# Performance work log

Measured on AMD Instinct MI355X. Metric: run time of the kernel, lower is better.

Reference implementation:

```python
import jax, jax.numpy as jnp
import numpy as np

D = 1024
H = 16
HD = D // H
EPS = 1e-6


def rms_norm(x, w):
    # x: [..., hd]; compute in float32 like the torch module
    xf = x.astype(jnp.float32)
    rms = jnp.sqrt(jnp.mean(xf * xf, axis=-1, keepdims=True) + EPS)
    return (xf / rms * w.astype(jnp.float32)).astype(x.dtype)


def setup_inputs() -> dict:
    key = jax.random.key(0)
    ks = jax.random.split(key, 6)
    B, S = 2, 2048
    x = jax.random.normal(ks[0], (B, S, D), dtype=jnp.float32)
    Wqkv = jax.random.normal(ks[1], (3 * D, D), dtype=jnp.float32) * (1.0 / np.sqrt(D))
    bqkv = jax.random.normal(ks[2], (3 * D,), dtype=jnp.float32) * 0.02
    Wproj = jax.random.normal(ks[3], (D, D), dtype=jnp.float32) * (1.0 / np.sqrt(D))
    bproj = jax.random.normal(ks[4], (D,), dtype=jnp.float32) * 0.02
    qn_w = jnp.ones((HD,), dtype=jnp.float32)
    kn_w = jnp.ones((HD,), dtype=jnp.float32)
    return {"x": x, "Wqkv": Wqkv, "bqkv": bqkv, "Wproj": Wproj, "bproj": bproj,
            "qn_w": qn_w, "kn_w": kn_w}


def reference(x, Wqkv, bqkv, Wproj, bproj, qn_w, kn_w):
    B, S, _ = x.shape
    # QKV projection: torch Linear is x @ W.T + b
    qkv = x @ Wqkv.T + bqkv                     # [B, S, 3D]
    qkv = qkv.reshape(B, S, 3, H, HD)
    q, k, v = qkv[:, :, 0], qkv[:, :, 1], qkv[:, :, 2]   # each [B, S, H, hd]
    q = rms_norm(q, qn_w)
    k = rms_norm(k, kn_w)
    # move heads forward: [B, H, S, hd]
    q = q.transpose(0, 2, 1, 3)
    k = k.transpose(0, 2, 1, 3)
    v = v.transpose(0, 2, 1, 3)
    scale = 1.0 / np.sqrt(HD)
    scores = jnp.einsum('bhsd,bhtd->bhst', q, k) * scale   # [B, H, S, S] (math backend)
    attn = jax.nn.softmax(scores, axis=-1)
    out = jnp.einsum('bhst,bhtd->bhsd', attn, v)            # [B, H, S, hd]
    out = out.transpose(0, 2, 1, 3).reshape(B, S, D)
    return out @ Wproj.T + bproj
```

## Files before the change

### kernel.cpp

```cpp
#include <hip/hip_runtime.h>
#include <hip/hip_bf16.h>
#include <math.h>

#define D_MODEL 1024
#define NH 16
#define HD 64
#define SEQ 2048
#define BATCH 2
#define NTOK (BATCH*SEQ)

typedef short bf16x8 __attribute__((ext_vector_type(8)));
typedef short s4 __attribute__((ext_vector_type(4)));
typedef float f32x4 __attribute__((ext_vector_type(4)));
typedef unsigned short us4 __attribute__((ext_vector_type(4)));

#define MFMA(a,b,c) __builtin_amdgcn_mfma_f32_16x16x32_bf16(a,b,c,0,0,0)

union bfu { __hip_bfloat16 b; unsigned short u; };
__device__ __forceinline__ unsigned short f2b(float f){ bfu t; t.b = __float2bfloat16(f); return t.u; }
__device__ __forceinline__ float b2f(unsigned short u){ bfu t; t.u = u; return __bfloat162float(t.b); }
__device__ __forceinline__ unsigned short f2bf(float f){
    unsigned int u = __float_as_uint(f);
    u += 0x7FFFu + ((u >> 16) & 1u);
    return (unsigned short)(u >> 16);
}

__device__ __forceinline__ void g2l16(const unsigned short* g, unsigned short* l){
    __builtin_amdgcn_global_load_lds(
        (const __attribute__((address_space(1))) unsigned int*)g,
        (__attribute__((address_space(3))) unsigned int*)l, 16, 0, 0);
}

#define OFF_X   128L
#define OFF_WQ  (OFF_X  + 4194304L)
#define OFF_BQ  (OFF_WQ + 3145728L)
#define OFF_WP  (OFF_BQ + 3072L)
#define OFF_BP  (OFF_WP + 1048576L)
#define OFF_QN  (OFF_BP + 1024L)
#define OFF_KN  (OFF_QN + 64L)
#define OFF_Q   (OFF_KN + 64L)
#define OFF_K   (OFF_Q  + 4194304L)
#define OFF_V   (OFF_K  + 4194304L)
#define OFF_A   (OFF_V  + 4194304L)


__global__ __launch_bounds__(256) void detect_kernel(
    const unsigned int* __restrict__ xraw, int* __restrict__ cnt)
{
    int i = blockIdx.x*256 + threadIdx.x;
    uint4 v = ((const uint4*)xraw)[i];
    unsigned int w[4] = {v.x, v.y, v.z, v.w};
    int local = 0;
    #pragma unroll
    for (int j=0;j<4;j++){
        local += ((w[j] & 0x7F80u) >= 0x4800u);
        local += (((w[j]>>16) & 0x7F80u) >= 0x4800u);
    }
    if (local) atomicAdd(cnt, local);
}

__global__ __launch_bounds__(256) void convert_kernel(
    const void* __restrict__ x,  const void* __restrict__ wq,
    const void* __restrict__ bq, const void* __restrict__ wp,
    const void* __restrict__ bp, const void* __restrict__ qn,
    const void* __restrict__ kn, unsigned short* __restrict__ ws,
    const int* __restrict__ cntp)
{
    const int flag = (*cntp > 256);
    long i = (long)blockIdx.x*blockDim.x + threadIdx.x;
    const long stride = (long)gridDim.x*blockDim.x;
    const long NCH = 2098208L;
    for (; i < NCH; i += stride){
        long j = i; const void* src; long off;
        if (j < 1048576L)                  { src = x;  off = OFF_X;  }
        else if ((j -= 1048576L) < 786432L){ src = wq; off = OFF_WQ; }
        else if ((j -= 786432L)  < 768L)   { src = bq; off = OFF_BQ; }
        else if ((j -= 768L)     < 262144L){ src = wp; off = OFF_WP; }
        else if ((j -= 262144L)  < 256L)   { src = bp; off = OFF_BP; }
        else if ((j -= 256L)     < 16L)    { src = qn; off = OFF_QN; }
        else      { j -= 16L;                src = kn; off = OFF_KN; }
        us4 o;
        if (flag){
            float4 v = ((const float4*)src)[j];
            o.x = f2b(v.x); o.y = f2b(v.y); o.z = f2b(v.z); o.w = f2b(v.w);
        } else {
            o = ((const us4*)src)[j];
        }
        *(us4*)(ws + off + j*4) = o;
    }
}

__global__ __launch_bounds__(256) void qkv_kernel(
    const unsigned short* __restrict__ x,
    const unsigned short* __restrict__ Wqkv,
    const unsigned short* __restrict__ bqkv,
    const unsigned short* __restrict__ qn_w,
    const unsigned short* __restrict__ kn_w,
    unsigned short* __restrict__ qbuf,
    unsigned short* __restrict__ kbuf,
    unsigned short* __restrict__ vbuf)
{
    __shared__ __align__(16) unsigned short tA[128*32];
    __shared__ __align__(16) unsigned short tB[128*32];
    const int tid  = threadIdx.x;
    const int w    = tid >> 6, lane = tid & 63, quad = lane >> 4, c = lane & 15;
    const int m0 = blockIdx.y*128, n0 = blockIdx.x*128;
    const int am = (w>>1)*64, bn = (w&1)*64;

    f32x4 acc[4][4];
    for (int mi=0;mi<4;mi++) for (int ni=0;ni<4;ni++) acc[mi][ni] = {0.f,0.f,0.f,0.f};

    const int i0 = tid, i1 = tid + 256;
    const long ga0 = (long)(m0 + (i0>>2))*D_MODEL + (i0&3)*8;
    const long ga1 = (long)(m0 + (i1>>2))*D_MODEL + (i1&3)*8;
    const long gb0 = (long)(n0 + (i0>>2))*D_MODEL + (i0&3)*8;
    const long gb1 = (long)(n0 + (i1>>2))*D_MODEL + (i1&3)*8;

    for (int k0=0;k0<D_MODEL;k0+=32){
        g2l16(x    + ga0 + k0, tA + i0*8);
        g2l16(x    + ga1 + k0, tA + i1*8);
        g2l16(Wqkv + gb0 + k0, tB + i0*8);
        g2l16(Wqkv + gb1 + k0, tB + i1*8);
        __syncthreads();
        bf16x8 a[4], b[4];
        for (int mi=0;mi<4;mi++) a[mi] = *(const bf16x8*)(tA + (am + mi*16 + c)*32 + quad*8);
        for (int ni=0;ni<4;ni++) b[ni] = *(const bf16x8*)(tB + (bn + ni*16 + c)*32 + quad*8);
        for (int mi=0;mi<4;mi++)
            for (int ni=0;ni<4;ni++)
                acc[mi][ni] = MFMA(a[mi], b[ni], acc[mi][ni]);
        __syncthreads();
    }

    const int nw = n0 + bn, mw = m0 + am;
    const int region = nw >> 10;
    const int h      = (nw & 1023) >> 6;
    float bias[4], wn[4];
    for (int ni=0;ni<4;ni++){
        bias[ni] = b2f(bqkv[nw + ni*16 + c]);
        wn[ni]   = 1.0f;
    }
    if (region==0) for (int ni=0;ni<4;ni++) wn[ni] = b2f(qn_w[ni*16+c]);
    if (region==1) for (int ni=0;ni<4;ni++) wn[ni] = b2f(kn_w[ni*16+c]);

    for (int mi=0;mi<4;mi++){
        for (int ni=0;ni<4;ni++)
            for (int r=0;r<4;r++) acc[mi][ni][r] += bias[ni];

        float scale_r[4];
        if (region < 2){
            for (int r=0;r<4;r++){
                float ss = 0.f;
                for (int ni=0;ni<4;ni++){ float v2 = acc[mi][ni][r]; ss += v2*v2; }
                ss += __shfl_xor(ss, 1, 64);
                ss += __shfl_xor(ss, 2, 64);
                ss += __shfl_xor(ss, 4, 64);
                ss += __shfl_xor(ss, 8, 64);
                scale_r[r] = rsqrtf(ss*(1.0f/64.0f) + 1e-6f);
            }
        } else {
            for (int r=0;r<4;r++) scale_r[r] = 1.0f;
        }

        for (int r=0;r<4;r++){
            int m = mw + mi*16 + quad*4 + r;
            int bidx = m >> 11, s = m & 2047;
            long bb = (long)(bidx*NH + h)*SEQ*HD;
            if (region == 0){
                long base = bb + (long)s*HD;
                for (int ni=0;ni<4;ni++)
                    qbuf[base + ni*16 + c] = f2bf(acc[mi][ni][r] * scale_r[r] * wn[ni]);
            } else if (region == 1){
                long tb = bb + (long)(s>>6)*4096;
                for (int ni=0;ni<4;ni++){
                    int d = ni*16 + c;
                    long idx = tb + (long)((s&63)*8 + ((d>>3) ^ (s&7)))*8 + (d&7);
                    kbuf[idx] = f2bf(acc[mi][ni][r] * scale_r[r] * wn[ni]);
                }
            } else {
                long tb = bb + (long)(s>>6)*4096;
                for (int ni=0;ni<4;ni++){
                    int d = ni*16 + c;
                    long idx = tb + (long)(d*8 + (((s>>3)&7) ^ (d&7)))*8 + (s&7);
                    vbuf[idx] = f2bf(acc[mi][ni][r]);
                }
            }
        }
    }
}

__global__ __launch_bounds__(256) void attn_kernel(
    const unsigned short* __restrict__ qbuf,
    const unsigned short* __restrict__ kts,
    const unsigned short* __restrict__ vts,
    unsigned short* __restrict__ abuf)
{
    const int tid = threadIdx.x, w = tid>>6, lane = tid&63, quad = lane>>4, c = lane&15;
    const int bh = blockIdx.y, qt = blockIdx.x;
    const unsigned short* qb = qbuf + (long)bh*SEQ*HD;
    const unsigned short* kb = kts + (long)bh*SEQ*HD;
    const unsigned short* vb = vts + (long)bh*SEQ*HD;
    const int qbase = qt*128 + w*32;
    const int cq = c & 7;

    __shared__ __align__(16) unsigned short KT[2][4096];
    __shared__ __align__(16) unsigned short VT[2][4096];
    __shared__ __align__(16) unsigned short P[4][2112];
    unsigned short* Pw = &P[w][0];

    bf16x8 aq[2][2];
    #pragma unroll
    for (int mi=0;mi<2;mi++)
        #pragma unroll
        for (int ks=0;ks<2;ks++)
            aq[mi][ks] = *(const bf16x8*)(qb + (long)(qbase + mi*16 + c)*HD + ks*32 + quad*8);

    f32x4 o[2][4];
    #pragma unroll
    for (int mi=0;mi<2;mi++)
        #pragma unroll
        for (int nt=0;nt<4;nt++) o[mi][nt] = {0.f,0.f,0.f,0.f};
    float l_loc[2] = {0.f, 0.f};

    auto stage = [&](const unsigned short* src, unsigned short* dst){
        g2l16(src + tid*8,        dst + tid*8);
        g2l16(src + 2048 + tid*8, dst + 2048 + tid*8);
    };

    stage(kb, KT[0]); stage(vb, VT[0]);
    __syncthreads();

    for (int kt2=0; kt2<SEQ/64; kt2++){
        const unsigned short* ktl = KT[kt2&1];
        const unsigned short* vtl = VT[kt2&1];
        if (kt2 < SEQ/64 - 1){
            stage(kb + (kt2+1)*4096, KT[(kt2&1)^1]);
            stage(vb + (kt2+1)*4096, VT[(kt2&1)^1]);
        }

        bf16x8 kf[4][2];
        #pragma unroll
        for (int mt=0;mt<4;mt++)
            #pragma unroll
            for (int ks=0;ks<2;ks++)
                kf[mt][ks] = *(const bf16x8*)(ktl + ((mt*16+c)*8 + ((ks*4+quad)^cq))*8);

        f32x4 z4[4][2];
        #pragma unroll
        for (int mt=0;mt<4;mt++)
            #pragma unroll
            for (int mi=0;mi<2;mi++){
                f32x4 t = {0.f,0.f,0.f,0.f};
                t = MFMA(kf[mt][0], aq[mi][0], t);
                t = MFMA(kf[mt][1], aq[mi][1], t);
                z4[mt][mi] = t;
            }

        #pragma unroll
        for (int mt=0;mt<4;mt++){
            const int key8 = mt*2 + (quad>>1);
            #pragma unroll
            for (int mi=0;mi<2;mi++){
                s4 pk;
                #pragma unroll
                for (int r=0;r<4;r++){
                    float p = exp2f(z4[mt][mi][r]*0.18033688f - 17.312340f);
                    l_loc[mi] += p;
                    pk[r] = (short)(__float_as_uint(p) >> 16);
                }
                *(s4*)(Pw + key8*264 + (mi*16+c)*8 + (quad&1)*4) = pk;
            }
        }

        #pragma unroll
        for (int ks=0;ks<2;ks++){
            bf16x8 bv[4];
            #pragma unroll
            for (int nt=0;nt<4;nt++)
                bv[nt] = *(const bf16x8*)(vtl + ((nt*16+c)*8 + ((ks*4+quad)^cq))*8);
            bf16x8 ap0 = *(const bf16x8*)(Pw + (ks*4+quad)*264 + c*8);
            bf16x8 ap1 = *(const bf16x8*)(Pw + (ks*4+quad)*264 + (16+c)*8);
            #pragma unroll
            for (int nt=0;nt<4;nt++){
                o[0][nt] = MFMA(ap0, bv[nt], o[0][nt]);
                o[1][nt] = MFMA(ap1, bv[nt], o[1][nt]);
            }
        }
        __syncthreads();
    }

    #pragma unroll
    for (int mi=0;mi<2;mi++){
        l_loc[mi] += __shfl_xor(l_loc[mi], 16, 64);
        l_loc[mi] += __shfl_xor(l_loc[mi], 32, 64);
    }

    const int b = bh >> 4, h = bh & 15;
    #pragma unroll
    for (int mi=0;mi<2;mi++)
        #pragma unroll
        for (int r=0;r<4;r++){
            float l = __shfl(l_loc[mi], quad*4 + r, 64);
            float inv = 1.0f / l;
            int s = qbase + mi*16 + quad*4 + r;
            long base = ((long)(b*SEQ + s)*NH + h)*HD;
            #pragma unroll
            for (int nt=0;nt<4;nt++)
                abuf[base + nt*16 + c] = f2bf(o[mi][nt][r]*inv);
        }
}

__global__ __launch_bounds__(256) void proj_kernel(
    const unsigned short* __restrict__ abuf,
    const unsigned short* __restrict__ Wp,
    const unsigned short* __restrict__ bp,
    void* __restrict__ outv,
    const int* __restrict__ cntp)
{
    __shared__ __align__(16) unsigned short tA[128*32];
    __shared__ __align__(16) unsigned short tB[64*32];
    const int tid  = threadIdx.x;
    const int w    = tid >> 6, lane = tid & 63, quad = lane >> 4, c = lane & 15;
    const int m0 = blockIdx.y*128, n0 = blockIdx.x*64;
    const int am = (w>>1)*64, bn = (w&1)*32;
    const int flag = (*cntp > 256);

    f32x4 acc[4][2];
    for (int mi=0;mi<4;mi++) for (int ni=0;ni<2;ni++) acc[mi][ni] = {0.f,0.f,0.f,0.f};

    const int i0 = tid, i1 = tid + 256;
    const long ga0 = (long)(m0 + (i0>>2))*D_MODEL + (i0&3)*8;
    const long ga1 = (long)(m0 + (i1>>2))*D_MODEL + (i1&3)*8;
    const long gb0 = (long)(n0 + (i0>>2))*D_MODEL + (i0&3)*8;

    for (int k0=0;k0<D_MODEL;k0+=32){
        g2l16(abuf + ga0 + k0, tA + i0*8);
        g2l16(abuf + ga1 + k0, tA + i1*8);
        g2l16(Wp   + gb0 + k0, tB + i0*8);
        __syncthreads();
        bf16x8 a[4], b[2];
        for (int mi=0;mi<4;mi++) a[mi] = *(const bf16x8*)(tA + (am + mi*16 + c)*32 + quad*8);
        for (int ni=0;ni<2;ni++) b[ni] = *(const bf16x8*)(tB + (bn + ni*16 + c)*32 + quad*8);
        for (int mi=0;mi<4;mi++)
            for (int ni=0;ni<2;ni++)
                acc[mi][ni] = MFMA(a[mi], b[ni], acc[mi][ni]);
        __syncthreads();
    }

    float bias[2];
    for (int ni=0;ni<2;ni++) bias[ni] = b2f(bp[n0 + bn + ni*16 + c]);

    for (int mi=0;mi<4;mi++)
        for (int r=0;r<4;r++){
            long m = m0 + am + mi*16 + quad*4 + r;
            for (int ni=0;ni<2;ni++){
                float val = acc[mi][ni][r] + bias[ni];
                long idx = m*D_MODEL + n0 + bn + ni*16 + c;
                if (flag) ((float*)outv)[idx] = val;
                else      ((unsigned short*)outv)[idx] = f2bf(val);
            }
        }
}

extern "C" void kernel_launch(void* const* d_in, const int* in_sizes, int n_in,
                              void* d_out, int out_size, void* d_ws, size_t ws_size,
                              hipStream_t stream)
{
    unsigned short* ws = (unsigned short*)d_ws;
    int* cnt = (int*)d_ws;

    hipMemsetAsync(cnt, 0, 4, stream);
    hipLaunchKernelGGL(detect_kernel, dim3(16), dim3(256), 0, stream,
                       (const unsigned int*)d_in[0], cnt);
    hipLaunchKernelGGL(convert_kernel, dim3(2048), dim3(256), 0, stream,
                       d_in[0], d_in[1], d_in[2], d_in[3], d_in[4], d_in[5], d_in[6],
                       ws, cnt);
    hipLaunchKernelGGL(qkv_kernel,  dim3(24,32), dim3(256), 0, stream,
                       ws+OFF_X, ws+OFF_WQ, ws+OFF_BQ, ws+OFF_QN, ws+OFF_KN,
                       ws+OFF_Q, ws+OFF_K, ws+OFF_V);
    hipLaunchKernelGGL(attn_kernel, dim3(16,32), dim3(256), 0, stream,
                       ws+OFF_Q, ws+OFF_K, ws+OFF_V, ws+OFF_A);
    hipLaunchKernelGGL(proj_kernel, dim3(16,32), dim3(256), 0, stream,
                       ws+OFF_A, ws+OFF_WP, ws+OFF_BP, d_out, cnt);
}
```

Baseline: 219.5 us.

## Keep softmax probabilities in registers via transposed QK and a re-laid-out V

The attention kernel now computes scores as K·Q so each lane's probabilities already sit in the MFMA B-operand layout for the PV product. This removes the per-warp LDS staging of P along with its writes, reads and bank traffic. V is stored by the QKV kernel in a new rotated layout so the PV operand can be assembled from two 8-byte LDS reads. The softmax scale is folded into the Q normalization weights, and the constant exp offset is dropped in favor of the raw exp2 intrinsic. Each warp now handles 16 query rows, the grid is doubled, and an occupancy hint is added, which trades more blocks re-staging K/V against lower register use per wave.

```diff
diff --git a/kernel.cpp b/kernel.cpp
--- a/kernel.cpp
+++ b/kernel.cpp
@@ -139,7 +139,7 @@
         bias[ni] = b2f(bqkv[nw + ni*16 + c]);
         wn[ni]   = 1.0f;
     }
-    if (region==0) for (int ni=0;ni<4;ni++) wn[ni] = b2f(qn_w[ni*16+c]);
+    if (region==0) for (int ni=0;ni<4;ni++) wn[ni] = b2f(qn_w[ni*16+c]) * 0.18033688f;
     if (region==1) for (int ni=0;ni<4;ni++) wn[ni] = b2f(kn_w[ni*16+c]);
 
     for (int mi=0;mi<4;mi++){
@@ -178,9 +178,13 @@
                 }
             } else {
                 long tb = bb + (long)(s>>6)*4096;
+                int ch2  = (s>>4)&3;
+                int fb   = ((s>>2)&3)*4;
+                int mloc = s&3;
                 for (int ni=0;ni<4;ni++){
                     int d = ni*16 + c;
-                    long idx = tb + (long)(d*8 + (((s>>3)&7) ^ (d&7)))*8 + (s&7);
+                    int f = fb + (((d>>1) + ch2)&3);
+                    long idx = tb + (long)d*64 + f*4 + mloc;
                     vbuf[idx] = f2bf(acc[mi][ni][r]);
                 }
             }
@@ -188,7 +192,7 @@
     }
 }
 
-__global__ __launch_bounds__(256) void attn_kernel(
+__global__ __launch_bounds__(256, 4) void attn_kernel(
     const unsigned short* __restrict__ qbuf,
     const unsigned short* __restrict__ kts,
     const unsigned short* __restrict__ vts,
@@ -199,27 +203,21 @@
     const unsigned short* qb = qbuf + (long)bh*SEQ*HD;
     const unsigned short* kb = kts + (long)bh*SEQ*HD;
     const unsigned short* vb = vts + (long)bh*SEQ*HD;
-    const int qbase = qt*128 + w*32;
+    const int qbase = qt*64 + w*16;
     const int cq = c & 7;
 
     __shared__ __align__(16) unsigned short KT[2][4096];
     __shared__ __align__(16) unsigned short VT[2][4096];
-    __shared__ __align__(16) unsigned short P[4][2112];
-    unsigned short* Pw = &P[w][0];
-
-    bf16x8 aq[2][2];
+
+    bf16x8 aq[2];
     #pragma unroll
-    for (int mi=0;mi<2;mi++)
-        #pragma unroll
-        for (int ks=0;ks<2;ks++)
-            aq[mi][ks] = *(const bf16x8*)(qb + (long)(qbase + mi*16 + c)*HD + ks*32 + quad*8);
-
-    f32x4 o[2][4];
+    for (int ks=0;ks<2;ks++)
+        aq[ks] = *(const bf16x8*)(qb + (long)(qbase + c)*HD + ks*32 + quad*8);
+
+    f32x4 o[4];
     #pragma unroll
-    for (int mi=0;mi<2;mi++)
-        #pragma unroll
-        for (int nt=0;nt<4;nt++) o[mi][nt] = {0.f,0.f,0.f,0.f};
-    float l_loc[2] = {0.f, 0.f};
+    for (int nt=0;nt<4;nt++) o[nt] = {0.f,0.f,0.f,0.f};
+    f32x4 l4 = {0.f,0.f,0.f,0.f};
 
     auto stage = [&](const unsigned short* src, unsigned short* dst){
         g2l16(src + tid*8,        dst + tid*8);
@@ -244,69 +242,62 @@
             for (int ks=0;ks<2;ks++)
                 kf[mt][ks] = *(const bf16x8*)(ktl + ((mt*16+c)*8 + ((ks*4+quad)^cq))*8);
 
-        f32x4 z4[4][2];
-        #pragma unroll
-        for (int mt=0;mt<4;mt++)
-            #pragma unroll
-            for (int mi=0;mi<2;mi++){
-                f32x4 t = {0.f,0.f,0.f,0.f};
-                t = MFMA(kf[mt][0], aq[mi][0], t);
-                t = MFMA(kf[mt][1], aq[mi][1], t);
-                z4[mt][mi] = t;
-            }
-
+        f32x4 z4[4];
         #pragma unroll
         for (int mt=0;mt<4;mt++){
-            const int key8 = mt*2 + (quad>>1);
-            #pragma unroll
-            for (int mi=0;mi<2;mi++){
-                s4 pk;
-                #pragma unroll
-                for (int r=0;r<4;r++){
-                    float p = exp2f(z4[mt][mi][r]*0.18033688f - 17.312340f);
-                    l_loc[mi] += p;
-                    pk[r] = (short)(__float_as_uint(p) >> 16);
-                }
-                *(s4*)(Pw + key8*264 + (mi*16+c)*8 + (quad&1)*4) = pk;
-            }
+            f32x4 t = {0.f,0.f,0.f,0.f};
+            t = MFMA(kf[mt][0], aq[0], t);
+            t = MFMA(kf[mt][1], aq[1], t);
+            z4[mt] = t;
+        }
+
+        unsigned int pk[4][2];
+        #pragma unroll
+        for (int mt=0;mt<4;mt++){
+            float p0 = __builtin_amdgcn_exp2f(z4[mt][0]);
+            float p1 = __builtin_amdgcn_exp2f(z4[mt][1]);
+            float p2 = __builtin_amdgcn_exp2f(z4[mt][2]);
+            float p3 = __builtin_amdgcn_exp2f(z4[mt][3]);
+            l4[0] += p0; l4[1] += p1; l4[2] += p2; l4[3] += p3;
+            pk[mt][0] = __builtin_amdgcn_perm(__float_as_uint(p1), __float_as_uint(p0), 0x07060302u);
+            pk[mt][1] = __builtin_amdgcn_perm(__float_as_uint(p3), __float_as_uint(p2), 0x07060302u);
         }
 
         #pragma unroll
         for (int ks=0;ks<2;ks++){
-            bf16x8 bv[4];
-            #pragma unroll
-            for (int nt=0;nt<4;nt++)
-                bv[nt] = *(const bf16x8*)(vtl + ((nt*16+c)*8 + ((ks*4+quad)^cq))*8);
-            bf16x8 ap0 = *(const bf16x8*)(Pw + (ks*4+quad)*264 + c*8);
-            bf16x8 ap1 = *(const bf16x8*)(Pw + (ks*4+quad)*264 + (16+c)*8);
+            union { unsigned int u[4]; bf16x8 v; } pB;
+            pB.u[0] = pk[2*ks][0];   pB.u[1] = pk[2*ks][1];
+            pB.u[2] = pk[2*ks+1][0]; pB.u[3] = pk[2*ks+1][1];
             #pragma unroll
             for (int nt=0;nt<4;nt++){
-                o[0][nt] = MFMA(ap0, bv[nt], o[0][nt]);
-                o[1][nt] = MFMA(ap1, bv[nt], o[1][nt]);
+                const int dv = nt*16 + c;
+                const unsigned short* vbase = vtl + dv*64;
+                int flo = quad*4 + (((dv>>1) + ks*2    )&3);
+                int fhi = quad*4 + (((dv>>1) + ks*2 + 1)&3);
+                uint2 lo = *(const uint2*)(vbase + flo*4);
+                uint2 hi = *(const uint2*)(vbase + fhi*4);
+                union { unsigned int u[4]; bf16x8 v; } vv;
+                vv.u[0]=lo.x; vv.u[1]=lo.y; vv.u[2]=hi.x; vv.u[3]=hi.y;
+                o[nt] = MFMA(vv.v, pB.v, o[nt]);
             }
         }
         __syncthreads();
     }
 
+    float l_loc = (l4[0]+l4[1]) + (l4[2]+l4[3]);
+    l_loc += __shfl_xor(l_loc, 16, 64);
+    l_loc += __shfl_xor(l_loc, 32, 64);
+    float inv = 1.0f / l_loc;
+
+    const int b = bh >> 4, h = bh & 15;
+    long base = ((long)(b*SEQ + qbase + c)*NH + h)*HD;
     #pragma unroll
-    for (int mi=0;mi<2;mi++){
-        l_loc[mi] += __shfl_xor(l_loc[mi], 16, 64);
-        l_loc[mi] += __shfl_xor(l_loc[mi], 32, 64);
-    }
-
-    const int b = bh >> 4, h = bh & 15;
-    #pragma unroll
-    for (int mi=0;mi<2;mi++)
-        #pragma unroll
-        for (int r=0;r<4;r++){
-            float l = __shfl(l_loc[mi], quad*4 + r, 64);
-            float inv = 1.0f / l;
-            int s = qbase + mi*16 + quad*4 + r;
-            long base = ((long)(b*SEQ + s)*NH + h)*HD;
-            #pragma unroll
-            for (int nt=0;nt<4;nt++)
-                abuf[base + nt*16 + c] = f2bf(o[mi][nt][r]*inv);
-        }
+    for (int nt=0;nt<4;nt++){
+        us4 pkd;
+        #pragma unroll
+        for (int r=0;r<4;r++) pkd[r] = f2bf(o[nt][r]*inv);
+        *(us4*)(abuf + base + nt*16 + quad*4) = pkd;
+    }
 }
 
 __global__ __launch_bounds__(256) void proj_kernel(
@@ -377,7 +368,7 @@
     hipLaunchKernelGGL(qkv_kernel,  dim3(24,32), dim3(256), 0, stream,
                        ws+OFF_X, ws+OFF_WQ, ws+OFF_BQ, ws+OFF_QN, ws+OFF_KN,
                        ws+OFF_Q, ws+OFF_K, ws+OFF_V);
-    hipLaunchKernelGGL(attn_kernel, dim3(16,32), dim3(256), 0, stream,
+    hipLaunchKernelGGL(attn_kernel, dim3(32,32), dim3(256), 0, stream,
                        ws+OFF_Q, ws+OFF_K, ws+OFF_V, ws+OFF_A);
     hipLaunchKernelGGL(proj_kernel, dim3(16,32), dim3(256), 0, stream,
                        ws+OFF_A, ws+OFF_WP, ws+OFF_BP, d_out, cnt);
```

Result: no change. 223.1 us (+1.6%).
